# Kernel tuning notes

Hardware: AMD Instinct MI355X
Metric: run time of the kernel (lower is better)

The kernel has to match this reference:

```python
import jax, jax.numpy as jnp
import numpy as np
import math

V, E, H, L, HID, T, B = 32000, 1024, 16, 4, 4096, 1024, 4
HS = E // H  # head size = 64


def _ln(x, g, b, eps=1e-5):
    m = jnp.mean(x, axis=-1, keepdims=True)
    v = jnp.var(x, axis=-1, keepdims=True)
    return (x - m) * jax.lax.rsqrt(v + eps) * g + b


def _pos_encoding(t, e):
    pos = jnp.arange(t, dtype=jnp.float32)[:, None]
    div = jnp.exp(jnp.arange(0, e, 2, dtype=jnp.float32) * (-math.log(10000.0) / e))
    pe = jnp.zeros((t, e), dtype=jnp.float32)
    pe = pe.at[:, 0::2].set(jnp.sin(pos * div))
    pe = pe.at[:, 1::2].set(jnp.cos(pos * div))
    return pe


def setup_inputs() -> dict:
    key = jax.random.key(0)
    ks = jax.random.split(key, 16)
    std = 0.02
    inp = {
        'idx': jax.random.randint(ks[0], (B, T), 0, V),
        'targets': jax.random.randint(ks[1], (B, T), 0, V),
        'tok_emb': jax.random.normal(ks[2], (V, E), jnp.float32) * std,
        'ln1_g': jnp.ones((L, E), jnp.float32),
        'ln1_b': jnp.zeros((L, E), jnp.float32),
        'wq': jax.random.normal(ks[3], (L, H, E, HS), jnp.float32) * std,
        'wk': jax.random.normal(ks[4], (L, H, E, HS), jnp.float32) * std,
        'wv': jax.random.normal(ks[5], (L, H, E, HS), jnp.float32) * std,
        'wo': jax.random.normal(ks[6], (L, H * HS, E), jnp.float32) * std,
        'bo': jnp.zeros((L, E), jnp.float32),
        'ln2_g': jnp.ones((L, E), jnp.float32),
        'ln2_b': jnp.zeros((L, E), jnp.float32),
        'w1': jax.random.normal(ks[7], (L, E, HID), jnp.float32) * std,
        'b1': jnp.zeros((L, HID), jnp.float32),
        'w2': jax.random.normal(ks[8], (L, HID, E), jnp.float32) * std,
        'b2': jnp.zeros((L, E), jnp.float32),
        'lnf_g': jnp.ones((E,), jnp.float32),
        'lnf_b': jnp.zeros((E,), jnp.float32),
        'lm_w': jax.random.normal(ks[9], (E, V), jnp.float32) * std,
        'lm_b': jnp.zeros((V,), jnp.float32),
    }
    return inp


def _forward(idx, targets, tok_emb, ln1_g, ln1_b, wq, wk, wv, wo, bo,
             ln2_g, ln2_b, w1, b1, w2, b2, lnf_g, lnf_b, lm_w, lm_b):
    b, t = idx.shape
    x = tok_emb[idx] * math.sqrt(E)              # [B,T,E], scaled embedding
    x = x + _pos_encoding(t, E)                  # sinusoidal pos enc
    causal = jnp.tril(jnp.ones((t, t), dtype=bool))
    scale = HS ** -0.5
    for l in range(L):
        h = _ln(x, ln1_g[l], ln1_b[l])
        q = jnp.einsum('bte,hek->bhtk', h, wq[l])
        k = jnp.einsum('bte,hek->bhtk', h, wk[l])
        v = jnp.einsum('bte,hek->bhtk', h, wv[l])
        scores = jnp.einsum('bhtk,bhsk->bhts', q, k) * scale
        scores = jnp.where(causal, scores, -jnp.inf)
        w = jax.nn.softmax(scores, axis=-1)
        o = jnp.einsum('bhts,bhsk->bhtk', w, v)
        o = o.transpose(0, 2, 1, 3).reshape(b, t, H * HS)  # concat heads
        x = x + o @ wo[l] + bo[l]
        h2 = _ln(x, ln2_g[l], ln2_b[l])
        x = x + jax.nn.relu(h2 @ w1[l] + b1[l]) @ w2[l] + b2[l]
    x = _ln(x, lnf_g, lnf_b)
    logits = x @ lm_w + lm_b                     # [B,T,V]
    logp = jax.nn.log_softmax(logits, axis=-1)
    loss = -jnp.mean(jnp.take_along_axis(logp, targets[..., None], axis=-1))
    return logits, loss


def reference(idx, targets, tok_emb, ln1_g, ln1_b, wq, wk, wv, wo, bo,
              ln2_g, ln2_b, w1, b1, w2, b2, lnf_g, lnf_b, lm_w, lm_b):
    return _forward(idx, targets, tok_emb, ln1_g, ln1_b, wq, wk, wv, wo, bo,
                    ln2_g, ln2_b, w1, b1, w2, b2, lnf_g, lnf_b, lm_w, lm_b)
```

## Files before the change

### kernel.cpp

```cpp
#include <hip/hip_runtime.h>
#include <hip/hip_bf16.h>
#include <math.h>

#define BB 4
#define TT 1024
#define BT 4096
#define EE 1024
#define HH 16
#define HSZ 64
#define LL 4
#define HID 4096
#define VV 32000
#define LOG2E 1.44269504f

typedef __attribute__((ext_vector_type(8))) __bf16 bf16x8;
typedef __attribute__((ext_vector_type(4))) float f32x4;

#define MFMA16(a, b, c) __builtin_amdgcn_mfma_f32_16x16x32_bf16((a), (b), (c), 0, 0, 0)

__device__ __forceinline__ int swz32(int row, int chunk) {
    return row * 32 + ((chunk ^ ((row >> 1) & 3)) << 3);
}

__device__ __forceinline__ void gload16(const __bf16* g, __bf16* l) {
    __builtin_amdgcn_global_load_lds(
        (const __attribute__((address_space(1))) unsigned int*)g,
        (__attribute__((address_space(3))) unsigned int*)l, 16, 0, 0);
}

#define BAR() do { asm volatile("" ::: "memory"); __builtin_amdgcn_s_barrier(); asm volatile("" ::: "memory"); } while (0)

__global__ __launch_bounds__(256) void transpose_conv(
    const float* __restrict__ in, __bf16* __restrict__ out,
    int R, int C, long ibs, int bdiv, long os1, long os2)
{
    __shared__ __bf16 tile[64][65];
    const int t = threadIdx.x;
    const int c0 = blockIdx.x * 64, r0 = blockIdx.y * 64;
    const int batch = blockIdx.z;
    const float* ib = in + (size_t)batch * ibs;
    __bf16* ob = out + (size_t)(batch / bdiv) * os1 + (size_t)(batch % bdiv) * os2;
#pragma unroll
    for (int p = 0; p < 4; ++p) {
        const int r = (t >> 4) + p * 16;
        const int c = (t & 15) * 4;
        float4 v = *(const float4*)(ib + (size_t)(r0 + r) * C + c0 + c);
        tile[c + 0][r] = (__bf16)v.x;
        tile[c + 1][r] = (__bf16)v.y;
        tile[c + 2][r] = (__bf16)v.z;
        tile[c + 3][r] = (__bf16)v.w;
    }
    __syncthreads();
#pragma unroll
    for (int p = 0; p < 2; ++p) {
        const int g = t + p * 256;
        const int co = g >> 3, ch = g & 7;
        bf16x8 vv;
#pragma unroll
        for (int j = 0; j < 8; ++j) vv[j] = tile[co][ch * 8 + j];
        *(bf16x8*)(ob + (size_t)(c0 + co) * R + r0 + ch * 8) = vv;
    }
}

__global__ __launch_bounds__(256) void embed_kernel(
    const int* __restrict__ idx, const float* __restrict__ emb, float* __restrict__ x)
{
    const int row = blockIdx.x, tid = threadIdx.x;
    const float pos = (float)(row & (TT - 1));
    const int tok = idx[row];
    const int cb = tid * 4;
    float4 ev = *(const float4*)(emb + (size_t)tok * EE + cb);
    const float kk = -9.2103403720f / (float)EE;
    float pe[4];
#pragma unroll
    for (int j = 0; j < 4; ++j) {
        const int c = cb + j;
        const float div = expf(kk * (float)(c & ~1));
        const float ang = pos * div;
        pe[j] = (c & 1) ? cosf(ang) : sinf(ang);
    }
    float4 r;
    r.x = ev.x * 32.0f + pe[0];
    r.y = ev.y * 32.0f + pe[1];
    r.z = ev.z * 32.0f + pe[2];
    r.w = ev.w * 32.0f + pe[3];
    *(float4*)(x + (size_t)row * EE + cb) = r;
}

__global__ __launch_bounds__(256) void ln_kernel(
    const float* __restrict__ x, const float* __restrict__ g,
    const float* __restrict__ be, __bf16* __restrict__ out)
{
    __shared__ float red[2][4];
    const int row = blockIdx.x, tid = threadIdx.x;
    float4 v = *(const float4*)(x + (size_t)row * EE + tid * 4);
    float s = v.x + v.y + v.z + v.w;
    float ss = v.x * v.x + v.y * v.y + v.z * v.z + v.w * v.w;
#pragma unroll
    for (int m = 1; m < 64; m <<= 1) { s += __shfl_xor(s, m); ss += __shfl_xor(ss, m); }
    if ((tid & 63) == 0) { red[0][tid >> 6] = s; red[1][tid >> 6] = ss; }
    __syncthreads();
    s  = red[0][0] + red[0][1] + red[0][2] + red[0][3];
    ss = red[1][0] + red[1][1] + red[1][2] + red[1][3];
    const float mean = s * (1.0f / EE);
    const float var  = ss * (1.0f / EE) - mean * mean;
    const float rs   = rsqrtf(var + 1e-5f);
    float4 gv = *(const float4*)(g + tid * 4);
    float4 bv = *(const float4*)(be + tid * 4);
    __bf16* o = out + (size_t)row * EE + tid * 4;
    o[0] = (__bf16)((v.x - mean) * rs * gv.x + bv.x);
    o[1] = (__bf16)((v.y - mean) * rs * gv.y + bv.y);
    o[2] = (__bf16)((v.z - mean) * rs * gv.z + bv.z);
    o[3] = (__bf16)((v.w - mean) * rs * gv.w + bv.w);
}

template <int MODE>
__global__ __launch_bounds__(512, 2) void gemm256(
    const __bf16* __restrict__ A, const __bf16* __restrict__ Bt,
    const float* __restrict__ bias, float* __restrict__ C,
    __bf16* __restrict__ Cb, float2* __restrict__ part,
    int M, int N, int K)
{
    __shared__ __bf16 As[2][2][256 * 32];
    __shared__ __bf16 Bs[2][2][256 * 32];
    __shared__ float2 lred[(MODE == 4) ? 256 : 1][(MODE == 4) ? 4 : 1];

    const int tid = threadIdx.x;
    const int lane = tid & 63, wid = tid >> 6;
    const int wm = wid >> 2, wn = wid & 3;
    const int nwg = gridDim.x;
    const int b = blockIdx.x;
    const int gj = (b & 7) * (nwg >> 3) + (b >> 3);
    const int bm = gj & 15, bn = gj >> 4;
    const int m0 = bm * 256, n0 = bn * 256;
    const int l15 = lane & 15, lg = lane >> 4;

    const int rl = (wid << 4) + (lane >> 2);
    const int cl = (lane & 3) ^ ((rl >> 1) & 3);
    const int ldso = (wid << 4) * 32;
    const size_t ga = (size_t)(m0 + rl) * K + cl * 8;
    const size_t gb = (size_t)(n0 + rl) * K + cl * 8;
    const size_t rowhK = (size_t)128 * K;

    auto stageA = [&](int buf, int kh, int kt) {
        const size_t go = (size_t)kt * 64 + (size_t)kh * 32;
        gload16(A + ga + go,         &As[buf][kh][ldso]);
        gload16(A + ga + rowhK + go, &As[buf][kh][4096 + ldso]);
    };
    auto stageB = [&](int buf, int kh, int kt) {
        const size_t go = (size_t)kt * 64 + (size_t)kh * 32;
        gload16(Bt + gb + go,         &Bs[buf][kh][ldso]);
        gload16(Bt + gb + rowhK + go, &Bs[buf][kh][4096 + ldso]);
    };

    f32x4 acc[8][4] = {};

    auto ldA = [&](bf16x8 (&af)[4], int cur, int kh, int qi) {
#pragma unroll
        for (int i = 0; i < 4; ++i)
            af[i] = *(const bf16x8*)(&As[cur][kh][swz32(wm * 128 + (qi * 4 + i) * 16 + l15, lg)]);
    };
    auto ldB = [&](bf16x8 (&bf)[4], int cur, int kh) {
#pragma unroll
        for (int j = 0; j < 4; ++j)
            bf[j] = *(const bf16x8*)(&Bs[cur][kh][swz32(wn * 64 + j * 16 + l15, lg)]);
    };
    auto mm = [&](bf16x8 (&af)[4], bf16x8 (&bf)[4], int qi) {
        __builtin_amdgcn_s_setprio(1);
#pragma unroll
        for (int i = 0; i < 4; ++i)
#pragma unroll
            for (int j = 0; j < 4; ++j)
                acc[qi * 4 + i][j] = MFMA16(af[i], bf[j], acc[qi * 4 + i][j]);
        __builtin_amdgcn_s_setprio(0);
    };

    const int nkt = K >> 6;

    stageB(0, 0, 0); stageA(0, 0, 0); stageB(0, 1, 0); stageA(0, 1, 0);
    stageB(1, 0, 1); stageA(1, 0, 1); stageB(1, 1, 1);
    asm volatile("s_waitcnt vmcnt(10)" ::: "memory");
    BAR();

    for (int g = 0; g < nkt; ++g) {
        const int cur = g & 1;
        const int kA1 = (g + 1 < nkt) ? g + 1 : nkt - 1;
        const int kN  = (g + 2 < nkt) ? g + 2 : nkt - 1;
        bf16x8 af[4], bf[4];
        ldA(af, cur, 0, 0); ldB(bf, cur, 0);
        stageA(cur ^ 1, 1, kA1);
        BAR();
        mm(af, bf, 0);
        BAR();
        ldA(af, cur, 0, 1);
        stageB(cur, 0, kN);
        asm volatile("s_waitcnt vmcnt(10)" ::: "memory");
        BAR();
        mm(af, bf, 1);
        BAR();
        ldA(af, cur, 1, 0); ldB(bf, cur, 1);
        stageA(cur, 0, kN);
        BAR();
        mm(af, bf, 0);
        BAR();
        ldA(af, cur, 1, 1);
        stageB(cur, 1, kN);
        asm volatile("s_waitcnt vmcnt(10)" ::: "memory");
        BAR();
        mm(af, bf, 1);
        BAR();
    }
    asm volatile("s_waitcnt vmcnt(0)" ::: "memory");

    const int crow = m0 + wm * 128;
    const int ccol = n0 + wn * 64 + l15;
#pragma unroll
    for (int fi = 0; fi < 8; ++fi)
#pragma unroll
        for (int j = 0; j < 4; ++j) {
            const int cc = ccol + j * 16;
#pragma unroll
            for (int r = 0; r < 4; ++r) {
                const size_t oidx = (size_t)(crow + fi * 16 + lg * 4 + r) * N + cc;
                float v = acc[fi][j][r];
                if (MODE == 0) {
                    Cb[oidx] = (__bf16)v;
                } else if (MODE == 1) {
                    v += bias[cc];
                    Cb[oidx] = (__bf16)(v > 0.0f ? v : 0.0f);
                } else {
                    C[oidx] = v + bias[cc];
                }
            }
        }

    if constexpr (MODE == 4) {
#pragma unroll
        for (int fi = 0; fi < 8; ++fi)
#pragma unroll
            for (int r = 0; r < 4; ++r) {
                float tv[4];
                float mx = -1e30f;
#pragma unroll
                for (int j = 0; j < 4; ++j) {
                    tv[j] = acc[fi][j][r] + bias[ccol + j * 16];
                    mx = fmaxf(mx, tv[j]);
                }
                mx = fmaxf(mx, __shfl_xor(mx, 1));
                mx = fmaxf(mx, __shfl_xor(mx, 2));
                mx = fmaxf(mx, __shfl_xor(mx, 4));
                mx = fmaxf(mx, __shfl_xor(mx, 8));
                float sm = 0.0f;
#pragma unroll
                for (int j = 0; j < 4; ++j) sm += exp2f((tv[j] - mx) * LOG2E);
                sm += __shfl_xor(sm, 1);
                sm += __shfl_xor(sm, 2);
                sm += __shfl_xor(sm, 4);
                sm += __shfl_xor(sm, 8);
                if (l15 == 0)
                    lred[wm * 128 + fi * 16 + lg * 4 + r][wn] = make_float2(mx, sm);
            }
        BAR();
        if (tid < 256) {
            float M2 = -1e30f;
#pragma unroll
            for (int w = 0; w < 4; ++w) M2 = fmaxf(M2, lred[tid][w].x);
            float S = 0.0f;
#pragma unroll
            for (int w = 0; w < 4; ++w) S += lred[tid][w].y * exp2f((lred[tid][w].x - M2) * LOG2E);
            part[(size_t)(m0 + tid) * (N >> 8) + bn] = make_float2(M2, S);
        }
    }
}

template <int MODE, int BN>
__global__ __launch_bounds__(256, 2) void gemm_bt(
    const __bf16* __restrict__ A, const __bf16* __restrict__ Bt,
    const float* __restrict__ bias, float* __restrict__ C,
    __bf16* __restrict__ Cb, int M, int N, int K)
{
    constexpr int JW  = BN / 32;
    constexpr int BSW = BN / 64;
    __shared__ __bf16 As[128 * 32];
    __shared__ __bf16 Bs[BN * 32];

    const int tid = threadIdx.x;
    const int lane = tid & 63, wid = tid >> 6;
    const int wr = wid >> 1, wc = wid & 1;
    const int m0 = blockIdx.y * 128, n0 = blockIdx.x * BN;

    size_t sA[2];  int loA[2];
#pragma unroll
    for (int c = 0; c < 2; ++c) {
        const int seg = wid * 2 + c;
        const int rl = seg * 16 + (lane >> 2);
        const int cl = (lane & 3) ^ ((rl >> 1) & 3);
        loA[c] = seg * 512;
        sA[c] = (size_t)(m0 + rl) * K + cl * 8;
    }
    size_t sB[BSW]; int loB[BSW];
#pragma unroll
    for (int c = 0; c < BSW; ++c) {
        const int seg = wid * BSW + c;
        const int rl = seg * 16 + (lane >> 2);
        const int cl = (lane & 3) ^ ((rl >> 1) & 3);
        loB[c] = seg * 512;
        sB[c] = (size_t)(n0 + rl) * K + cl * 8;
    }

    const int l15 = lane & 15, kch = lane >> 4;
    const int abase = swz32(wr * 64 + l15, kch);
    const int bbase = swz32(wc * (BN / 2) + l15, kch);

    f32x4 acc[4][JW] = {};

    const int nk = K >> 5;
    for (int kt = 0; kt < nk; ++kt) {
        const size_t ko = (size_t)kt * 32;
#pragma unroll
        for (int c = 0; c < 2; ++c)   gload16(A + sA[c] + ko, As + loA[c]);
#pragma unroll
        for (int c = 0; c < BSW; ++c) gload16(Bt + sB[c] + ko, Bs + loB[c]);
        __syncthreads();
        bf16x8 af[4], bfr[JW];
#pragma unroll
        for (int i = 0; i < 4; ++i)  af[i]  = *(const bf16x8*)(As + abase + i * 512);
#pragma unroll
        for (int j = 0; j < JW; ++j) bfr[j] = *(const bf16x8*)(Bs + bbase + j * 512);
#pragma unroll
        for (int i = 0; i < 4; ++i)
#pragma unroll
            for (int j = 0; j < JW; ++j)
                acc[i][j] = MFMA16(af[i], bfr[j], acc[i][j]);
        __syncthreads();
    }

    const int crow = m0 + wr * 64 + ((lane >> 4) << 2);
    const int ccol = n0 + wc * (BN / 2) + l15;
#pragma unroll
    for (int i = 0; i < 4; ++i)
#pragma unroll
        for (int j = 0; j < JW; ++j) {
            const int cc = ccol + j * 16;
#pragma unroll
            for (int r = 0; r < 4; ++r) {
                const size_t oidx = (size_t)(crow + i * 16 + r) * N + cc;
                float v = acc[i][j][r];
                if (MODE == 0) {
                    Cb[oidx] = (__bf16)v;
                } else if (MODE == 1) {
                    v += bias[cc];
                    Cb[oidx] = (__bf16)(v > 0.0f ? v : 0.0f);
                } else if (MODE == 2) {
                    C[oidx] += v + bias[cc];
                } else {
                    C[oidx] = v + bias[cc];
                }
            }
        }
}

__global__ __launch_bounds__(64) void attn_kernel(
    const __bf16* __restrict__ qkv, __bf16* __restrict__ out)
{
    __shared__ __bf16 Pl[16 * 32];
    __shared__ __bf16 Vt[64 * 32];
    const int lane = threadIdx.x;
    const int bh = blockIdx.x, b = bh >> 4, hh = bh & 15;
    const int qbase = blockIdx.y * 16;
    const int RS = 3 * EE;
    const __bf16* qp = qkv + (size_t)(b * TT) * RS + hh * HSZ;
    const __bf16* kp = qp + EE;
    const __bf16* vp = qp + 2 * EE;
    const int l15 = lane & 15, lg = lane >> 4;

    bf16x8 aq[2];
#pragma unroll
    for (int e = 0; e < 2; ++e)
        aq[e] = *(const bf16x8*)(qp + (size_t)(qbase + l15) * RS + e * 32 + lg * 8);

    f32x4 ao[4] = {};
    float mrun[4], lrun[4];
#pragma unroll
    for (int r = 0; r < 4; ++r) { mrun[r] = -1e30f; lrun[r] = 0.0f; }

    const int ntile = qbase / 32 + 1;
    for (int st = 0; st < ntile; ++st) {
        const int sbase = st * 32;
        f32x4 as[2] = {};
        __builtin_amdgcn_s_setprio(1);
#pragma unroll
        for (int n = 0; n < 2; ++n)
#pragma unroll
            for (int e = 0; e < 2; ++e) {
                bf16x8 bk = *(const bf16x8*)(kp + (size_t)(sbase + n * 16 + l15) * RS + e * 32 + lg * 8);
                as[n] = MFMA16(aq[e], bk, as[n]);
            }
        __builtin_amdgcn_s_setprio(0);
        {
            const int sl = lane >> 1;
            const int e0 = (lane & 1) * 32;
            const __bf16* vr = vp + (size_t)(sbase + sl) * RS + e0;
#pragma unroll
            for (int c = 0; c < 4; ++c) {
                bf16x8 vvv = *(const bf16x8*)(vr + c * 8);
#pragma unroll
                for (int j = 0; j < 8; ++j)
                    Vt[swz32(e0 + c * 8 + j, sl >> 3) + (sl & 7)] = vvv[j];
            }
        }
#pragma unroll
        for (int r = 0; r < 4; ++r) {
            const int qi = qbase + lg * 4 + r;
            float sc0 = as[0][r] * 0.125f;
            float sc1 = as[1][r] * 0.125f;
            if (sbase + l15 > qi)      sc0 = -1e30f;
            if (sbase + 16 + l15 > qi) sc1 = -1e30f;
            float rm = fmaxf(sc0, sc1);
            rm = fmaxf(rm, __shfl_xor(rm, 1));
            rm = fmaxf(rm, __shfl_xor(rm, 2));
            rm = fmaxf(rm, __shfl_xor(rm, 4));
            rm = fmaxf(rm, __shfl_xor(rm, 8));
            const float mnew = fmaxf(mrun[r], rm);
            const float alpha = exp2f((mrun[r] - mnew) * LOG2E);
            const float p0 = exp2f((sc0 - mnew) * LOG2E);
            const float p1 = exp2f((sc1 - mnew) * LOG2E);
            float rs = p0 + p1;
            rs += __shfl_xor(rs, 1);
            rs += __shfl_xor(rs, 2);
            rs += __shfl_xor(rs, 4);
            rs += __shfl_xor(rs, 8);
            lrun[r] = lrun[r] * alpha + rs;
            mrun[r] = mnew;
#pragma unroll
            for (int n = 0; n < 4; ++n) ao[n][r] *= alpha;
            const int prow = lg * 4 + r;
            Pl[swz32(prow, l15 >> 3) + (l15 & 7)] = (__bf16)p0;
            Pl[swz32(prow, (16 + l15) >> 3) + (l15 & 7)] = (__bf16)p1;
        }
        asm volatile("s_waitcnt lgkmcnt(0)" ::: "memory");
        bf16x8 pa = *(const bf16x8*)(&Pl[swz32(l15, lg)]);
        __builtin_amdgcn_s_setprio(1);
#pragma unroll
        for (int n = 0; n < 4; ++n) {
            bf16x8 bv = *(const bf16x8*)(&Vt[swz32(n * 16 + l15, lg)]);
            ao[n] = MFMA16(pa, bv, ao[n]);
        }
        __builtin_amdgcn_s_setprio(0);
        asm volatile("s_waitcnt lgkmcnt(0)" ::: "memory");
    }
#pragma unroll
    for (int r = 0; r < 4; ++r) {
        const float inv = 1.0f / lrun[r];
        const int row = qbase + lg * 4 + r;
#pragma unroll
        for (int n = 0; n < 4; ++n)
            out[(size_t)(b * TT + row) * EE + hh * HSZ + n * 16 + l15] =
                (__bf16)(ao[n][r] * inv);
    }
}

__global__ __launch_bounds__(256) void loss_reduce(
    const float2* __restrict__ part, const float* __restrict__ logits,
    const int* __restrict__ tgt, float* __restrict__ lossv, int NP)
{
    __shared__ float rm[4], rs2[4];
    const int row = blockIdx.x, tid = threadIdx.x;
    float m = -1e30f, s = 0.0f;
    if (tid < NP) {
        const float2 p = part[(size_t)row * NP + tid];
        m = p.x; s = p.y;
    }
#pragma unroll
    for (int k = 1; k < 64; k <<= 1) {
        const float mo = __shfl_xor(m, k), so = __shfl_xor(s, k);
        const float mn = fmaxf(m, mo);
        s = s * exp2f((m - mn) * LOG2E) + so * exp2f((mo - mn) * LOG2E);
        m = mn;
    }
    if ((tid & 63) == 0) { rm[tid >> 6] = m; rs2[tid >> 6] = s; }
    __syncthreads();
    if (tid == 0) {
        float M = rm[0];
#pragma unroll
        for (int w = 1; w < 4; ++w) M = fmaxf(M, rm[w]);
        float S = 0.0f;
#pragma unroll
        for (int w = 0; w < 4; ++w) S += rs2[w] * exp2f((rm[w] - M) * LOG2E);
        lossv[row] = M + logf(S) - logits[(size_t)row * VV + tgt[row]];
    }
}

__global__ __launch_bounds__(256) void loss_final(const float* __restrict__ lossv, float* __restrict__ out)
{
    __shared__ float red[4];
    const int tid = threadIdx.x;
    float s = 0.0f;
    for (int i = tid; i < BT; i += 256) s += lossv[i];
#pragma unroll
    for (int k = 1; k < 64; k <<= 1) s += __shfl_xor(s, k);
    if ((tid & 63) == 0) red[tid >> 6] = s;
    __syncthreads();
    if (tid == 0) out[0] = (red[0] + red[1] + red[2] + red[3]) * (1.0f / BT);
}

extern "C" void kernel_launch(void* const* d_in, const int* in_sizes, int n_in,
                              void* d_out, int out_size, void* d_ws, size_t ws_size,
                              hipStream_t stream)
{
    const int*   idx   = (const int*)d_in[0];
    const int*   tgt   = (const int*)d_in[1];
    const float* temb  = (const float*)d_in[2];
    const float* ln1g  = (const float*)d_in[3];
    const float* ln1b  = (const float*)d_in[4];
    const float* wq    = (const float*)d_in[5];
    const float* wk    = (const float*)d_in[6];
    const float* wv    = (const float*)d_in[7];
    const float* wo    = (const float*)d_in[8];
    const float* bo    = (const float*)d_in[9];
    const float* ln2g  = (const float*)d_in[10];
    const float* ln2b  = (const float*)d_in[11];
    const float* w1    = (const float*)d_in[12];
    const float* b1    = (const float*)d_in[13];
    const float* w2    = (const float*)d_in[14];
    const float* b2    = (const float*)d_in[15];
    const float* lnfg  = (const float*)d_in[16];
    const float* lnfb  = (const float*)d_in[17];
    const float* lm_w  = (const float*)d_in[18];
    const float* lm_b  = (const float*)d_in[19];

    float* logits  = (float*)d_out;
    float* lossout = logits + (size_t)BT * VV;

    char* ws = (char*)d_ws;
    size_t off = 0;
    auto carve = [&](size_t bytes) {
        void* p = ws + off;
        off += (bytes + 255) & ~(size_t)255;
        return p;
    };
    __bf16* WQKVT = (__bf16*)carve((size_t)LL * 3072 * 1024 * 2);
    __bf16* WOT   = (__bf16*)carve((size_t)LL * 1024 * 1024 * 2);
    __bf16* W1T   = (__bf16*)carve((size_t)LL * 4096 * 1024 * 2);
    __bf16* W2T   = (__bf16*)carve((size_t)LL * 1024 * 4096 * 2);
    __bf16* LMT   = (__bf16*)carve((size_t)VV * 1024 * 2);
    float*  x     = (float*)carve((size_t)BT * EE * 4);
    __bf16* h     = (__bf16*)carve((size_t)BT * EE * 2);
    __bf16* qkv   = (__bf16*)carve((size_t)BT * 3072 * 2);
    __bf16* mid   = (__bf16*)carve((size_t)BT * HID * 2);
    float*  lossv = (float*)carve((size_t)BT * 4);
    float2* part  = (float2*)mid;

    const dim3 blk(256);

    transpose_conv<<<dim3(1, 16, 64), blk, 0, stream>>>(wq, WQKVT,           1024, 64,   65536, 16, 3145728, 65536);
    transpose_conv<<<dim3(1, 16, 64), blk, 0, stream>>>(wk, WQKVT + 1048576, 1024, 64,   65536, 16, 3145728, 65536);
    transpose_conv<<<dim3(1, 16, 64), blk, 0, stream>>>(wv, WQKVT + 2097152, 1024, 64,   65536, 16, 3145728, 65536);
    transpose_conv<<<dim3(16, 16, 4), blk, 0, stream>>>(wo, WOT,   1024, 1024, 1048576, 4, 0, 1048576);
    transpose_conv<<<dim3(64, 16, 4), blk, 0, stream>>>(w1, W1T,   1024, 4096, 4194304, 4, 0, 4194304);
    transpose_conv<<<dim3(16, 64, 4), blk, 0, stream>>>(w2, W2T,   4096, 1024, 4194304, 4, 0, 4194304);
    transpose_conv<<<dim3(500, 16, 1), blk, 0, stream>>>(lm_w, LMT, 1024, 32000, 0, 1, 0, 0);

    embed_kernel<<<BT, blk, 0, stream>>>(idx, temb, x);

    for (int l = 0; l < LL; ++l) {
        ln_kernel<<<BT, blk, 0, stream>>>(x, ln1g + l * EE, ln1b + l * EE, h);
        gemm256<0><<<dim3(192), dim3(512), 0, stream>>>(h, WQKVT + (size_t)l * 3145728,
                                                        nullptr, nullptr, qkv, nullptr, BT, 3072, 1024);
        attn_kernel<<<dim3(64, 64), dim3(64), 0, stream>>>(qkv, h);
        gemm_bt<2, 64><<<dim3(16, 32), blk, 0, stream>>>(h, WOT + (size_t)l * 1048576,
                                                         bo + l * EE, x, nullptr, BT, 1024, 1024);
        ln_kernel<<<BT, blk, 0, stream>>>(x, ln2g + l * EE, ln2b + l * EE, h);
        gemm256<1><<<dim3(256), dim3(512), 0, stream>>>(h, W1T + (size_t)l * 4194304,
                                                        b1 + l * HID, nullptr, mid, nullptr, BT, 4096, 1024);
        gemm_bt<2, 64><<<dim3(16, 32), blk, 0, stream>>>(mid, W2T + (size_t)l * 4194304,
                                                         b2 + l * EE, x, nullptr, BT, 1024, 4096);
    }
    ln_kernel<<<BT, blk, 0, stream>>>(x, lnfg, lnfb, h);
    gemm256<4><<<dim3(2000), dim3(512), 0, stream>>>(h, LMT, lm_b, logits, nullptr, part, BT, VV, 1024);
    loss_reduce<<<BT, blk, 0, stream>>>(part, logits, tgt, lossv, VV >> 8);
    loss_final<<<1, blk, 0, stream>>>(lossv, lossout);
}
```

Measured before the change: 1.808 ms.

## Restrict 256-tile GEMM to LM head; rework its pipeline and block mapping

The 256x256 GEMM is now used only for the LM-head logits and loss partials. Its K-loop is restructured into a simpler double-buffered schedule: the next tile is prefetched one step ahead with a single vmcnt wait per sub-stage, and blocks map to tiles through an XCD-aware scheme. The QKV and FFN-up projections move to the smaller 128-wide gemm_bt kernel, which gives more blocks and better occupancy for those shapes. The costs are a shallower prefetch depth in the big GEMM and possibly lower per-block efficiency for the moved projections.

```diff
diff --git a/kernel.cpp b/kernel.cpp
--- a/kernel.cpp
+++ b/kernel.cpp
@@ -28,7 +28,7 @@
         (__attribute__((address_space(3))) unsigned int*)l, 16, 0, 0);
 }
 
-#define BAR() do { asm volatile("" ::: "memory"); __builtin_amdgcn_s_barrier(); asm volatile("" ::: "memory"); } while (0)
+#define FENCE() asm volatile("" ::: "memory")
 
 __global__ __launch_bounds__(256) void transpose_conv(
     const float* __restrict__ in, __bf16* __restrict__ out,
@@ -114,165 +114,6 @@
     o[3] = (__bf16)((v.w - mean) * rs * gv.w + bv.w);
 }
 
-template <int MODE>
-__global__ __launch_bounds__(512, 2) void gemm256(
-    const __bf16* __restrict__ A, const __bf16* __restrict__ Bt,
-    const float* __restrict__ bias, float* __restrict__ C,
-    __bf16* __restrict__ Cb, float2* __restrict__ part,
-    int M, int N, int K)
-{
-    __shared__ __bf16 As[2][2][256 * 32];
-    __shared__ __bf16 Bs[2][2][256 * 32];
-    __shared__ float2 lred[(MODE == 4) ? 256 : 1][(MODE == 4) ? 4 : 1];
-
-    const int tid = threadIdx.x;
-    const int lane = tid & 63, wid = tid >> 6;
-    const int wm = wid >> 2, wn = wid & 3;
-    const int nwg = gridDim.x;
-    const int b = blockIdx.x;
-    const int gj = (b & 7) * (nwg >> 3) + (b >> 3);
-    const int bm = gj & 15, bn = gj >> 4;
-    const int m0 = bm * 256, n0 = bn * 256;
-    const int l15 = lane & 15, lg = lane >> 4;
-
-    const int rl = (wid << 4) + (lane >> 2);
-    const int cl = (lane & 3) ^ ((rl >> 1) & 3);
-    const int ldso = (wid << 4) * 32;
-    const size_t ga = (size_t)(m0 + rl) * K + cl * 8;
-    const size_t gb = (size_t)(n0 + rl) * K + cl * 8;
-    const size_t rowhK = (size_t)128 * K;
-
-    auto stageA = [&](int buf, int kh, int kt) {
-        const size_t go = (size_t)kt * 64 + (size_t)kh * 32;
-        gload16(A + ga + go,         &As[buf][kh][ldso]);
-        gload16(A + ga + rowhK + go, &As[buf][kh][4096 + ldso]);
-    };
-    auto stageB = [&](int buf, int kh, int kt) {
-        const size_t go = (size_t)kt * 64 + (size_t)kh * 32;
-        gload16(Bt + gb + go,         &Bs[buf][kh][ldso]);
-        gload16(Bt + gb + rowhK + go, &Bs[buf][kh][4096 + ldso]);
-    };
-
-    f32x4 acc[8][4] = {};
-
-    auto ldA = [&](bf16x8 (&af)[4], int cur, int kh, int qi) {
-#pragma unroll
-        for (int i = 0; i < 4; ++i)
-            af[i] = *(const bf16x8*)(&As[cur][kh][swz32(wm * 128 + (qi * 4 + i) * 16 + l15, lg)]);
-    };
-    auto ldB = [&](bf16x8 (&bf)[4], int cur, int kh) {
-#pragma unroll
-        for (int j = 0; j < 4; ++j)
-            bf[j] = *(const bf16x8*)(&Bs[cur][kh][swz32(wn * 64 + j * 16 + l15, lg)]);
-    };
-    auto mm = [&](bf16x8 (&af)[4], bf16x8 (&bf)[4], int qi) {
-        __builtin_amdgcn_s_setprio(1);
-#pragma unroll
-        for (int i = 0; i < 4; ++i)
-#pragma unroll
-            for (int j = 0; j < 4; ++j)
-                acc[qi * 4 + i][j] = MFMA16(af[i], bf[j], acc[qi * 4 + i][j]);
-        __builtin_amdgcn_s_setprio(0);
-    };
-
-    const int nkt = K >> 6;
-
-    stageB(0, 0, 0); stageA(0, 0, 0); stageB(0, 1, 0); stageA(0, 1, 0);
-    stageB(1, 0, 1); stageA(1, 0, 1); stageB(1, 1, 1);
-    asm volatile("s_waitcnt vmcnt(10)" ::: "memory");
-    BAR();
-
-    for (int g = 0; g < nkt; ++g) {
-        const int cur = g & 1;
-        const int kA1 = (g + 1 < nkt) ? g + 1 : nkt - 1;
-        const int kN  = (g + 2 < nkt) ? g + 2 : nkt - 1;
-        bf16x8 af[4], bf[4];
-        ldA(af, cur, 0, 0); ldB(bf, cur, 0);
-        stageA(cur ^ 1, 1, kA1);
-        BAR();
-        mm(af, bf, 0);
-        BAR();
-        ldA(af, cur, 0, 1);
-        stageB(cur, 0, kN);
-        asm volatile("s_waitcnt vmcnt(10)" ::: "memory");
-        BAR();
-        mm(af, bf, 1);
-        BAR();
-        ldA(af, cur, 1, 0); ldB(bf, cur, 1);
-        stageA(cur, 0, kN);
-        BAR();
-        mm(af, bf, 0);
-        BAR();
-        ldA(af, cur, 1, 1);
-        stageB(cur, 1, kN);
-        asm volatile("s_waitcnt vmcnt(10)" ::: "memory");
-        BAR();
-        mm(af, bf, 1);
-        BAR();
-    }
-    asm volatile("s_waitcnt vmcnt(0)" ::: "memory");
-
-    const int crow = m0 + wm * 128;
-    const int ccol = n0 + wn * 64 + l15;
-#pragma unroll
-    for (int fi = 0; fi < 8; ++fi)
-#pragma unroll
-        for (int j = 0; j < 4; ++j) {
-            const int cc = ccol + j * 16;
-#pragma unroll
-            for (int r = 0; r < 4; ++r) {
-                const size_t oidx = (size_t)(crow + fi * 16 + lg * 4 + r) * N + cc;
-                float v = acc[fi][j][r];
-                if (MODE == 0) {
-                    Cb[oidx] = (__bf16)v;
-                } else if (MODE == 1) {
-                    v += bias[cc];
-                    Cb[oidx] = (__bf16)(v > 0.0f ? v : 0.0f);
-                } else {
-                    C[oidx] = v + bias[cc];
-                }
-            }
-        }
-
-    if constexpr (MODE == 4) {
-#pragma unroll
-        for (int fi = 0; fi < 8; ++fi)
-#pragma unroll
-            for (int r = 0; r < 4; ++r) {
-                float tv[4];
-                float mx = -1e30f;
-#pragma unroll
-                for (int j = 0; j < 4; ++j) {
-                    tv[j] = acc[fi][j][r] + bias[ccol + j * 16];
-                    mx = fmaxf(mx, tv[j]);
-                }
-                mx = fmaxf(mx, __shfl_xor(mx, 1));
-                mx = fmaxf(mx, __shfl_xor(mx, 2));
-                mx = fmaxf(mx, __shfl_xor(mx, 4));
-                mx = fmaxf(mx, __shfl_xor(mx, 8));
-                float sm = 0.0f;
-#pragma unroll
-                for (int j = 0; j < 4; ++j) sm += exp2f((tv[j] - mx) * LOG2E);
-                sm += __shfl_xor(sm, 1);
-                sm += __shfl_xor(sm, 2);
-                sm += __shfl_xor(sm, 4);
-                sm += __shfl_xor(sm, 8);
-                if (l15 == 0)
-                    lred[wm * 128 + fi * 16 + lg * 4 + r][wn] = make_float2(mx, sm);
-            }
-        BAR();
-        if (tid < 256) {
-            float M2 = -1e30f;
-#pragma unroll
-            for (int w = 0; w < 4; ++w) M2 = fmaxf(M2, lred[tid][w].x);
-            float S = 0.0f;
-#pragma unroll
-            for (int w = 0; w < 4; ++w) S += lred[tid][w].y * exp2f((lred[tid][w].x - M2) * LOG2E);
-            part[(size_t)(m0 + tid) * (N >> 8) + bn] = make_float2(M2, S);
-        }
-    }
-}
-
 template <int MODE, int BN>
 __global__ __launch_bounds__(256, 2) void gemm_bt(
     const __bf16* __restrict__ A, const __bf16* __restrict__ Bt,
@@ -358,6 +199,141 @@
                 }
             }
         }
+}
+
+template <int MODE>
+__global__ __launch_bounds__(512, 2) void gemm256(
+    const __bf16* __restrict__ A, const __bf16* __restrict__ Bt,
+    const float* __restrict__ bias, float* __restrict__ C,
+    float2* __restrict__ part, int M, int N, int K)
+{
+    __shared__ __bf16 As[2][2][256 * 32];
+    __shared__ __bf16 Bs[2][2][256 * 32];
+    __shared__ float2 red[(MODE == 4) ? 256 : 1][(MODE == 4) ? 4 : 1];
+
+    const int tid = threadIdx.x;
+    const int lane = tid & 63, wid = tid >> 6;
+    const int wm = wid >> 2, wn = wid & 3;
+    const int jb = blockIdx.x >> 3, xcd = blockIdx.x & 7;
+    const int bm = xcd * 2 + (jb & 1);
+    const int bn = jb >> 1;
+    const int m0 = bm * 256, n0 = bn * 256;
+    const int l15 = lane & 15, lg = lane >> 4;
+
+    int ldso[2];
+    size_t ga[2], gb[2];
+#pragma unroll
+    for (int c = 0; c < 2; ++c) {
+        const int rl = c * 128 + wid * 16 + (lane >> 2);
+        const int cl = (lane & 3) ^ ((rl >> 1) & 3);
+        ldso[c] = (c * 128 + wid * 16) * 32;
+        ga[c] = (size_t)(m0 + rl) * K + cl * 8;
+        gb[c] = (size_t)(n0 + rl) * K + cl * 8;
+    }
+    auto stageA = [&](int buf, int kh, int kt) {
+        const size_t go = (size_t)kt * 64 + kh * 32;
+        gload16(A + ga[0] + go, &As[buf][kh][ldso[0]]);
+        gload16(A + ga[1] + go, &As[buf][kh][ldso[1]]);
+    };
+    auto stageB = [&](int buf, int kh, int kt) {
+        const size_t go = (size_t)kt * 64 + kh * 32;
+        gload16(Bt + gb[0] + go, &Bs[buf][kh][ldso[0]]);
+        gload16(Bt + gb[1] + go, &Bs[buf][kh][ldso[1]]);
+    };
+
+    f32x4 acc[8][4] = {};
+    const int nkt = K >> 6;
+
+    stageA(0, 0, 0); stageB(0, 0, 0); stageA(0, 1, 0); stageB(0, 1, 0);
+    asm volatile("s_waitcnt vmcnt(4)" ::: "memory");
+    FENCE(); __builtin_amdgcn_s_barrier(); FENCE();
+
+    for (int T = 0; T < nkt; ++T) {
+        const int b = T & 1;
+        const int kn = (T + 1 < nkt) ? T + 1 : nkt - 1;
+#pragma unroll
+        for (int kh = 0; kh < 2; ++kh) {
+            bf16x8 bfr[4];
+#pragma unroll
+            for (int qi = 0; qi < 2; ++qi) {
+                bf16x8 af[4];
+#pragma unroll
+                for (int i = 0; i < 4; ++i)
+                    af[i] = *(const bf16x8*)(&As[b][kh][swz32(wm * 128 + (qi * 4 + i) * 16 + l15, lg)]);
+                if (qi == 0) {
+#pragma unroll
+                    for (int j = 0; j < 4; ++j)
+                        bfr[j] = *(const bf16x8*)(&Bs[b][kh][swz32(wn * 64 + j * 16 + l15, lg)]);
+                    stageA(b ^ 1, kh, kn);
+                } else {
+                    stageB(b ^ 1, kh, kn);
+                }
+                __builtin_amdgcn_s_setprio(1);
+#pragma unroll
+                for (int i = 0; i < 4; ++i)
+#pragma unroll
+                    for (int j = 0; j < 4; ++j)
+                        acc[qi * 4 + i][j] = MFMA16(af[i], bfr[j], acc[qi * 4 + i][j]);
+                __builtin_amdgcn_s_setprio(0);
+                if (qi == 1)
+                    asm volatile("s_waitcnt vmcnt(4)" ::: "memory");
+                FENCE(); __builtin_amdgcn_s_barrier(); FENCE();
+            }
+        }
+    }
+    asm volatile("s_waitcnt vmcnt(0)" ::: "memory");
+
+    const int crow = m0 + wm * 128;
+    const int ccol = n0 + wn * 64 + l15;
+#pragma unroll
+    for (int fi = 0; fi < 8; ++fi)
+#pragma unroll
+        for (int j = 0; j < 4; ++j) {
+            const int cc = ccol + j * 16;
+#pragma unroll
+            for (int r = 0; r < 4; ++r) {
+                const size_t oidx = (size_t)(crow + fi * 16 + lg * 4 + r) * N + cc;
+                C[oidx] = acc[fi][j][r] + bias[cc];
+            }
+        }
+
+    if constexpr (MODE == 4) {
+#pragma unroll
+        for (int fi = 0; fi < 8; ++fi)
+#pragma unroll
+            for (int r = 0; r < 4; ++r) {
+                float tv[4];
+                float mx = -1e30f;
+#pragma unroll
+                for (int j = 0; j < 4; ++j) {
+                    tv[j] = acc[fi][j][r] + bias[ccol + j * 16];
+                    mx = fmaxf(mx, tv[j]);
+                }
+                mx = fmaxf(mx, __shfl_xor(mx, 1));
+                mx = fmaxf(mx, __shfl_xor(mx, 2));
+                mx = fmaxf(mx, __shfl_xor(mx, 4));
+                mx = fmaxf(mx, __shfl_xor(mx, 8));
+                float sm = 0.0f;
+#pragma unroll
+                for (int j = 0; j < 4; ++j) sm += exp2f((tv[j] - mx) * LOG2E);
+                sm += __shfl_xor(sm, 1);
+                sm += __shfl_xor(sm, 2);
+                sm += __shfl_xor(sm, 4);
+                sm += __shfl_xor(sm, 8);
+                if (l15 == 0)
+                    red[wm * 128 + fi * 16 + lg * 4 + r][wn] = make_float2(mx, sm);
+            }
+        __syncthreads();
+        if (tid < 256) {
+            float M2 = -1e30f;
+#pragma unroll
+            for (int w = 0; w < 4; ++w) M2 = fmaxf(M2, red[tid][w].x);
+            float S = 0.0f;
+#pragma unroll
+            for (int w = 0; w < 4; ++w) S += red[tid][w].y * exp2f((red[tid][w].x - M2) * LOG2E);
+            part[(size_t)(m0 + tid) * (N >> 8) + bn] = make_float2(M2, S);
+        }
+    }
 }
 
 __global__ __launch_bounds__(64) void attn_kernel(
@@ -565,19 +541,19 @@
 
     for (int l = 0; l < LL; ++l) {
         ln_kernel<<<BT, blk, 0, stream>>>(x, ln1g + l * EE, ln1b + l * EE, h);
-        gemm256<0><<<dim3(192), dim3(512), 0, stream>>>(h, WQKVT + (size_t)l * 3145728,
-                                                        nullptr, nullptr, qkv, nullptr, BT, 3072, 1024);
+        gemm_bt<0, 128><<<dim3(24, 32), blk, 0, stream>>>(h, WQKVT + (size_t)l * 3145728,
+                                                          nullptr, nullptr, qkv, BT, 3072, 1024);
         attn_kernel<<<dim3(64, 64), dim3(64), 0, stream>>>(qkv, h);
         gemm_bt<2, 64><<<dim3(16, 32), blk, 0, stream>>>(h, WOT + (size_t)l * 1048576,
                                                          bo + l * EE, x, nullptr, BT, 1024, 1024);
         ln_kernel<<<BT, blk, 0, stream>>>(x, ln2g + l * EE, ln2b + l * EE, h);
-        gemm256<1><<<dim3(256), dim3(512), 0, stream>>>(h, W1T + (size_t)l * 4194304,
-                                                        b1 + l * HID, nullptr, mid, nullptr, BT, 4096, 1024);
+        gemm_bt<1, 128><<<dim3(32, 32), blk, 0, stream>>>(h, W1T + (size_t)l * 4194304,
+                                                          b1 + l * HID, nullptr, mid, BT, 4096, 1024);
         gemm_bt<2, 64><<<dim3(16, 32), blk, 0, stream>>>(mid, W2T + (size_t)l * 4194304,
                                                          b2 + l * EE, x, nullptr, BT, 1024, 4096);
     }
     ln_kernel<<<BT, blk, 0, stream>>>(x, lnfg, lnfb, h);
-    gemm256<4><<<dim3(2000), dim3(512), 0, stream>>>(h, LMT, lm_b, logits, nullptr, part, BT, VV, 1024);
+    gemm256<4><<<dim3(2000), dim3(512), 0, stream>>>(h, LMT, lm_b, logits, part, BT, VV, 1024);
     loss_reduce<<<BT, blk, 0, stream>>>(part, logits, tgt, lossv, VV >> 8);
     loss_final<<<1, blk, 0, stream>>>(lossv, lossout);
 }
```

Measured after the change: 1.729 ms. 1.05x faster.
